# Kernel optimization log

Hardware: AMD Instinct MI355X
Metric: run time of the kernel (lower is better)

## Reference

```python
import jax, jax.numpy as jnp
import numpy as np

N = 100_000   # nodes
E = 1_280_000 # edges
F_IN = 64
HID = 64

def setup_inputs() -> dict:
    key = jax.random.key(0)
    ks = jax.random.split(key, 5)
    x = jax.random.normal(ks[0], (N, F_IN), dtype=jnp.float32)
    edge_index = jax.random.randint(ks[1], (2, E), 0, N, dtype=jnp.int32)
    edge_weight = jax.random.uniform(ks[2], (E,), dtype=jnp.float32)
    s1 = 1.0 / np.sqrt(F_IN)
    W1 = jax.random.uniform(ks[3], (F_IN, HID), minval=-s1, maxval=s1, dtype=jnp.float32)
    b1 = jnp.zeros((HID,), jnp.float32)
    s2 = 1.0 / np.sqrt(HID)
    W2 = jax.random.uniform(ks[4], (HID, 1), minval=-s2, maxval=s2, dtype=jnp.float32)
    b2 = jnp.zeros((1,), jnp.float32)
    return {"x": x, "edge_index": edge_index, "edge_weight": edge_weight,
            "W1": W1, "b1": b1, "W2": W2, "b2": b2}


def reference(x, edge_index, edge_weight, W1, b1, W2, b2):
    # eval mode: edge dropout and feature dropout are identity.
    # GCNConv with add_self_loops=True: A_hat = A + I, D_hat^-1/2 A_hat D_hat^-1/2.
    row, col = edge_index[0], edge_index[1]
    sl = jnp.arange(N, dtype=row.dtype)
    row = jnp.concatenate([row, sl])
    col = jnp.concatenate([col, sl])
    w = jnp.concatenate([edge_weight, jnp.ones((N,), edge_weight.dtype)])
    # symmetric normalization (shared by both conv layers)
    deg = jax.ops.segment_sum(w, col, num_segments=N)          # [N]
    dinv = jnp.where(deg > 0, jax.lax.rsqrt(deg), 0.0)
    norm = dinv[row] * w * dinv[col]                           # [E+N]

    def gcn(h):  # h: [N, d] already linearly transformed
        msg = h[row] * norm[:, None]                           # gather + scale
        return jax.ops.segment_sum(msg, col, num_segments=N)   # scatter-add

    h = gcn(x @ W1) + b1          # conv1
    h = jax.nn.relu(h)            # relu (dropout = identity in eval)
    out = gcn(h @ W2) + b2        # conv2 -> [N, 1]
    return out
```

## Files before the change

kernel.cpp:

```cpp
#include <hip/hip_runtime.h>
#include <hip/hip_fp16.h>

#define CNT_SHIFT 26
#define DEG_MASK  ((1u << CNT_SHIFT) - 1)
#define DEG_SCALE 1048576.0f
#define CAP 8192
#define GSTRIDE 16

typedef __attribute__((ext_vector_type(8))) short short8;
typedef __attribute__((ext_vector_type(4))) float v4f;

__device__ __forceinline__ unsigned short f_to_h16(float f) {
    return __half_as_ushort(__float2half(f));
}
__device__ __forceinline__ float h16_to_f(unsigned short u) {
    return __half2float(__ushort_as_half(u));
}
__device__ __forceinline__ unsigned short f_to_bf16(float f) {
    unsigned int u = __float_as_uint(f);
    u += 0x7fffu + ((u >> 16) & 1u);
    return (unsigned short)(u >> 16);
}
__device__ __forceinline__ unsigned long long mkrec(int r, int c, float wv) {
    return (unsigned long long)r | ((unsigned long long)(c & 511) << 17)
         | ((unsigned long long)f_to_h16(wv) << 26);
}

__global__ __launch_bounds__(256) void k_scatter_gemm(
        const int4* __restrict__ row4, const int4* __restrict__ col4, const float4* __restrict__ w4,
        const int* __restrict__ row, const int* __restrict__ col, const float* __restrict__ w,
        unsigned* __restrict__ gcur, unsigned long long* __restrict__ binrec,
        const float* __restrict__ x, const float* __restrict__ W1,
        char* __restrict__ h1q, float* __restrict__ scales,
        int E4, int rem, int nBlkE, int nGemm, int n, int nbkt) {
    __shared__ int h[256];
    int blk = blockIdx.x, t = threadIdx.x;
    if (blk < nBlkE) {
        h[t] = 0;
        __syncthreads();
        int base = blk * 1024;
#pragma unroll
        for (int k = 0; k < 4; ++k) {
            int g = base + k * 256 + t;
            if (g < E4) {
                int4 c = col4[g];
                atomicAdd(&h[c.x >> 9], 1);
                atomicAdd(&h[c.y >> 9], 1);
                atomicAdd(&h[c.z >> 9], 1);
                atomicAdd(&h[c.w >> 9], 1);
            }
        }
        if (blk == 0 && t < rem) atomicAdd(&h[col[4 * E4 + t] >> 9], 1);
        __syncthreads();
        if (t < nbkt) {
            int bb = t + (blk % nbkt);
            bb -= (bb >= nbkt) ? nbkt : 0;
            int cnt = h[bb];
            int runbase = 0;
            if (cnt > 0) runbase = (int)atomicAdd(&gcur[(size_t)bb * GSTRIDE], (unsigned)cnt);
            h[bb] = bb * CAP + runbase;
        }
        __syncthreads();
#pragma unroll
        for (int k = 0; k < 4; ++k) {
            int g = base + k * 256 + t;
            if (g < E4) {
                int4   r = row4[g];
                int4   c = col4[g];
                float4 v = w4[g];
                { int pos = atomicAdd(&h[c.x >> 9], 1); binrec[pos] = mkrec(r.x, c.x, v.x); }
                { int pos = atomicAdd(&h[c.y >> 9], 1); binrec[pos] = mkrec(r.y, c.y, v.y); }
                { int pos = atomicAdd(&h[c.z >> 9], 1); binrec[pos] = mkrec(r.z, c.z, v.z); }
                { int pos = atomicAdd(&h[c.w >> 9], 1); binrec[pos] = mkrec(r.w, c.w, v.w); }
            }
        }
        if (blk == 0 && t < rem) {
            int e = 4 * E4 + t;
            int c = col[e];
            int pos = atomicAdd(&h[c >> 9], 1);
            binrec[pos] = mkrec(row[e], c, w[e]);
        }
    } else {
        int b = blk - nBlkE;
        int lane = t & 63;
        int wave = t >> 6;
        int q   = lane >> 4;
        int n16 = lane & 15;
        short8 bf[8];
#pragma unroll
        for (int ct = 0; ct < 4; ++ct) {
#pragma unroll
            for (int hh = 0; hh < 2; ++hh) {
                short8 v;
#pragma unroll
                for (int j = 0; j < 8; ++j)
                    v[j] = (short)f_to_bf16(W1[(hh * 32 + q * 8 + j) * 64 + ct * 16 + n16]);
                bf[ct * 2 + hh] = v;
            }
        }
        int ntile = (n + 15) >> 4;
        int stride = nGemm * 4;
        for (int tile = b * 4 + wave; tile < ntile; tile += stride) {
            int base = tile << 4;
            short8 a0, a1;
            if (base + 16 <= n) {
                const float* xr = x + (size_t)(base + n16) * 64 + q * 8;
                float4 u0 = *(const float4*)(xr);
                float4 u1 = *(const float4*)(xr + 4);
                float4 u2 = *(const float4*)(xr + 32);
                float4 u3 = *(const float4*)(xr + 36);
                a0[0] = (short)f_to_bf16(u0.x); a0[1] = (short)f_to_bf16(u0.y);
                a0[2] = (short)f_to_bf16(u0.z); a0[3] = (short)f_to_bf16(u0.w);
                a0[4] = (short)f_to_bf16(u1.x); a0[5] = (short)f_to_bf16(u1.y);
                a0[6] = (short)f_to_bf16(u1.z); a0[7] = (short)f_to_bf16(u1.w);
                a1[0] = (short)f_to_bf16(u2.x); a1[1] = (short)f_to_bf16(u2.y);
                a1[2] = (short)f_to_bf16(u2.z); a1[3] = (short)f_to_bf16(u2.w);
                a1[4] = (short)f_to_bf16(u3.x); a1[5] = (short)f_to_bf16(u3.y);
                a1[6] = (short)f_to_bf16(u3.z); a1[7] = (short)f_to_bf16(u3.w);
            } else {
                bool ok = (base + n16) < n;
                const float* xr = x + (size_t)(ok ? (base + n16) : 0) * 64 + q * 8;
#pragma unroll
                for (int j = 0; j < 8; ++j) {
                    a0[j] = ok ? (short)f_to_bf16(xr[j])      : (short)0;
                    a1[j] = ok ? (short)f_to_bf16(xr[32 + j]) : (short)0;
                }
            }
            v4f acc0 = {0.f, 0.f, 0.f, 0.f}, acc1 = acc0, acc2 = acc0, acc3 = acc0;
            acc0 = __builtin_amdgcn_mfma_f32_16x16x32_bf16(a0, bf[0], acc0, 0, 0, 0);
            acc0 = __builtin_amdgcn_mfma_f32_16x16x32_bf16(a1, bf[1], acc0, 0, 0, 0);
            acc1 = __builtin_amdgcn_mfma_f32_16x16x32_bf16(a0, bf[2], acc1, 0, 0, 0);
            acc1 = __builtin_amdgcn_mfma_f32_16x16x32_bf16(a1, bf[3], acc1, 0, 0, 0);
            acc2 = __builtin_amdgcn_mfma_f32_16x16x32_bf16(a0, bf[4], acc2, 0, 0, 0);
            acc2 = __builtin_amdgcn_mfma_f32_16x16x32_bf16(a1, bf[5], acc2, 0, 0, 0);
            acc3 = __builtin_amdgcn_mfma_f32_16x16x32_bf16(a0, bf[6], acc3, 0, 0, 0);
            acc3 = __builtin_amdgcn_mfma_f32_16x16x32_bf16(a1, bf[7], acc3, 0, 0, 0);
#pragma unroll
            for (int r = 0; r < 4; ++r) {
                int rowg = base + q * 4 + r;
                if (rowg >= n) break;
                float m = fmaxf(fmaxf(fabsf(acc0[r]), fabsf(acc1[r])),
                                fmaxf(fabsf(acc2[r]), fabsf(acc3[r])));
                m = fmaxf(m, __shfl_xor(m, 1, 64));
                m = fmaxf(m, __shfl_xor(m, 2, 64));
                m = fmaxf(m, __shfl_xor(m, 4, 64));
                m = fmaxf(m, __shfl_xor(m, 8, 64));
                m = fmaxf(m, 1e-20f);
                float inv = 127.0f / m;
                char* dst = h1q + (size_t)rowg * 64 + n16;
                dst[0]  = (char)__float2int_rn(acc0[r] * inv);
                dst[16] = (char)__float2int_rn(acc1[r] * inv);
                dst[32] = (char)__float2int_rn(acc2[r] * inv);
                dst[48] = (char)__float2int_rn(acc3[r] * inv);
                if (n16 == 0) scales[rowg] = m * (1.0f / 127.0f);
            }
        }
    }
}

__global__ __launch_bounds__(256) void k_bucket(
        const unsigned long long* __restrict__ binrec, const unsigned* __restrict__ gcur,
        float* __restrict__ dinv, int* __restrict__ off, int* __restrict__ bktend,
        unsigned* __restrict__ ep, float* __restrict__ scales,
        int N, int nbkt) {
    __shared__ unsigned cnt[512];
    __shared__ int   loff[512];
    __shared__ int   ssum[256];
    int b = blockIdx.x, t = threadIdx.x;
    int e0 = b * CAP;
    int tot = (int)gcur[(size_t)b * GSTRIDE];
    int e1 = e0 + tot;
    cnt[t] = 0u; cnt[t + 256] = 0u;
    __syncthreads();
    unsigned epw[32];
    unsigned crk[32];
#pragma unroll
    for (int k = 0; k < 32; ++k) {
        int i = e0 + t + k * 256;
        if (i < e1) {
            unsigned long long rec = binrec[i];
            int cl = (int)((rec >> 17) & 511);
            unsigned hb = (unsigned)((rec >> 26) & 0xFFFF);
            float wv = h16_to_f((unsigned short)hb);
            unsigned old = atomicAdd(&cnt[cl],
                                     (1u << CNT_SHIFT) + (unsigned)(wv * DEG_SCALE + 0.5f));
            unsigned rank = old >> CNT_SHIFT;
            epw[k] = ((unsigned)(rec & 0x1FFFF) << 15) | (hb & 0x7fffu);
            crk[k] = ((unsigned)cl << 16) | rank;
        }
    }
    __syncthreads();
    unsigned p0 = cnt[2 * t], p1 = cnt[2 * t + 1];
    int c0 = (int)(p0 >> CNT_SHIFT), c1 = (int)(p1 >> CNT_SHIFT);
    float d0 = rsqrtf((float)(p0 & DEG_MASK) * (1.0f / DEG_SCALE) + 1.0f);
    float d1 = rsqrtf((float)(p1 & DEG_MASK) * (1.0f / DEG_SCALE) + 1.0f);
    int ps = c0 + c1;
    ssum[t] = ps;
    __syncthreads();
    for (int o = 1; o < 256; o <<= 1) {
        int v = (t >= o) ? ssum[t - o] : 0;
        __syncthreads();
        ssum[t] += v;
        __syncthreads();
    }
    int excl = ssum[t] - ps;
    loff[2 * t] = excl;
    loff[2 * t + 1] = excl + c0;
    int id0 = (b << 9) + 2 * t, id1 = id0 + 1;
    if (id0 < N) { dinv[id0] = d0; scales[id0] *= d0; off[id0] = e0 + excl; }
    if (id1 < N) { dinv[id1] = d1; scales[id1] *= d1; off[id1] = e0 + excl + c0; }
    if (t == 0) bktend[b] = e1;
    __syncthreads();
#pragma unroll
    for (int k = 0; k < 32; ++k) {
        int i = e0 + t + k * 256;
        if (i < e1) {
            int cl   = (int)(crk[k] >> 16);
            int rank = (int)(crk[k] & 0xFFFFu);
            ep[e0 + loff[cl] + rank] = epw[k];
        }
    }
}

__global__ __launch_bounds__(256) void k_agg1(
        const char* __restrict__ h1q, const float* __restrict__ scales,
        const int* __restrict__ off, const int* __restrict__ bktend,
        const unsigned* __restrict__ ep,
        const float* __restrict__ dinv, const float* __restrict__ b1,
        const float* __restrict__ W2,
        float* __restrict__ h2, int n) {
    int lane = threadIdx.x & 63;
    int wave = threadIdx.x >> 6;
    int grp  = lane >> 4;
    int fl   = (lane & 15) * 4;
    int i = blockIdx.x * 4 + wave;
    if (i >= n) return;
    float di = dinv[i];
    float4 acc;
    {
        char4 q4 = *(const char4*)(h1q + (size_t)i * 64 + fl);
        float si = (grp == 0) ? scales[i] : 0.f;
        acc.x = (float)q4.x * si;
        acc.y = (float)q4.y * si;
        acc.z = (float)q4.z * si;
        acc.w = (float)q4.w * si;
    }
    int s = off[i];
    int s1 = (((i & 511) == 511) || (i == n - 1)) ? bktend[i >> 9] : off[i + 1];
    for (; s + 8 <= s1; s += 8) {
        unsigned ea = ep[s + grp];
        unsigned eb = ep[s + 4 + grp];
        const char4 qa = *(const char4*)(h1q + (size_t)(ea >> 15) * 64 + fl);
        const char4 qb = *(const char4*)(h1q + (size_t)(eb >> 15) * 64 + fl);
        float ma = scales[ea >> 15] * h16_to_f((unsigned short)(ea & 0x7fff));
        float mb = scales[eb >> 15] * h16_to_f((unsigned short)(eb & 0x7fff));
        acc.x = fmaf((float)qa.x, ma, acc.x);
        acc.y = fmaf((float)qa.y, ma, acc.y);
        acc.z = fmaf((float)qa.z, ma, acc.z);
        acc.w = fmaf((float)qa.w, ma, acc.w);
        acc.x = fmaf((float)qb.x, mb, acc.x);
        acc.y = fmaf((float)qb.y, mb, acc.y);
        acc.z = fmaf((float)qb.z, mb, acc.z);
        acc.w = fmaf((float)qb.w, mb, acc.w);
    }
    for (; s < s1; s += 4) {
        int idx = s + grp;
        int sI = (idx < s1) ? idx : (s1 - 1);
        unsigned e = ep[sI];
        float m = (idx < s1) ? scales[e >> 15] * h16_to_f((unsigned short)(e & 0x7fff)) : 0.f;
        const char4 q4 = *(const char4*)(h1q + (size_t)(e >> 15) * 64 + fl);
        acc.x = fmaf((float)q4.x, m, acc.x);
        acc.y = fmaf((float)q4.y, m, acc.y);
        acc.z = fmaf((float)q4.z, m, acc.z);
        acc.w = fmaf((float)q4.w, m, acc.w);
    }
    acc.x += __shfl_xor(acc.x, 16, 64); acc.x += __shfl_xor(acc.x, 32, 64);
    acc.y += __shfl_xor(acc.y, 16, 64); acc.y += __shfl_xor(acc.y, 32, 64);
    acc.z += __shfl_xor(acc.z, 16, 64); acc.z += __shfl_xor(acc.z, 32, 64);
    acc.w += __shfl_xor(acc.w, 16, 64); acc.w += __shfl_xor(acc.w, 32, 64);
    float4 bb = *(const float4*)(b1 + fl);
    float4 ww = *(const float4*)(W2 + fl);
    float p = fmaxf(fmaf(di, acc.x, bb.x), 0.f) * ww.x
            + fmaxf(fmaf(di, acc.y, bb.y), 0.f) * ww.y
            + fmaxf(fmaf(di, acc.z, bb.z), 0.f) * ww.z
            + fmaxf(fmaf(di, acc.w, bb.w), 0.f) * ww.w;
#pragma unroll
    for (int o = 1; o < 16; o <<= 1) p += __shfl_xor(p, o, 64);
    if (lane == 0) h2[i] = di * p;
}

__global__ void k_agg2(const float* __restrict__ h2,
                       const int* __restrict__ off, const int* __restrict__ bktend,
                       const unsigned* __restrict__ ep, const float* __restrict__ dinv,
                       const float* __restrict__ b2, float* __restrict__ out, int n) {
    int i = blockIdx.x * 256 + threadIdx.x;
    if (i >= n) return;
    float acc = h2[i];
    int s = off[i];
    int s1 = (((i & 511) == 511) || (i == n - 1)) ? bktend[i >> 9] : off[i + 1];
    for (; s + 8 <= s1; s += 8) {
        unsigned e0 = ep[s],     e1 = ep[s + 1], e2 = ep[s + 2], e3 = ep[s + 3];
        unsigned e4 = ep[s + 4], e5 = ep[s + 5], e6 = ep[s + 6], e7 = ep[s + 7];
        float v0 = h2[e0 >> 15], v1 = h2[e1 >> 15], v2 = h2[e2 >> 15], v3 = h2[e3 >> 15];
        float v4 = h2[e4 >> 15], v5 = h2[e5 >> 15], v6 = h2[e6 >> 15], v7 = h2[e7 >> 15];
        acc = fmaf(v0, h16_to_f((unsigned short)(e0 & 0x7fff)), acc);
        acc = fmaf(v1, h16_to_f((unsigned short)(e1 & 0x7fff)), acc);
        acc = fmaf(v2, h16_to_f((unsigned short)(e2 & 0x7fff)), acc);
        acc = fmaf(v3, h16_to_f((unsigned short)(e3 & 0x7fff)), acc);
        acc = fmaf(v4, h16_to_f((unsigned short)(e4 & 0x7fff)), acc);
        acc = fmaf(v5, h16_to_f((unsigned short)(e5 & 0x7fff)), acc);
        acc = fmaf(v6, h16_to_f((unsigned short)(e6 & 0x7fff)), acc);
        acc = fmaf(v7, h16_to_f((unsigned short)(e7 & 0x7fff)), acc);
    }
    for (; s + 4 <= s1; s += 4) {
        unsigned e0 = ep[s], e1 = ep[s + 1], e2 = ep[s + 2], e3 = ep[s + 3];
        float v0 = h2[e0 >> 15], v1 = h2[e1 >> 15], v2 = h2[e2 >> 15], v3 = h2[e3 >> 15];
        acc = fmaf(v0, h16_to_f((unsigned short)(e0 & 0x7fff)), acc);
        acc = fmaf(v1, h16_to_f((unsigned short)(e1 & 0x7fff)), acc);
        acc = fmaf(v2, h16_to_f((unsigned short)(e2 & 0x7fff)), acc);
        acc = fmaf(v3, h16_to_f((unsigned short)(e3 & 0x7fff)), acc);
    }
    for (; s < s1; ++s) {
        unsigned e = ep[s];
        acc = fmaf(h2[e >> 15], h16_to_f((unsigned short)(e & 0x7fff)), acc);
    }
    out[i] = dinv[i] * acc + b2[0];
}

extern "C" void kernel_launch(void* const* d_in, const int* in_sizes, int n_in,
                              void* d_out, int out_size, void* d_ws, size_t ws_size,
                              hipStream_t stream) {
    const float* x  = (const float*)d_in[0];
    const int*   ei = (const int*)d_in[1];
    const float* w  = (const float*)d_in[2];
    const float* W1 = (const float*)d_in[3];
    const float* b1 = (const float*)d_in[4];
    const float* W2 = (const float*)d_in[5];
    const float* b2 = (const float*)d_in[6];
    float* out = (float*)d_out;

    const int N = in_sizes[0] / 64;
    const int E = in_sizes[2];
    const int* row = ei;
    const int* col = ei + E;

    const int nbkt  = (N + 511) >> 9;
    const int E4    = E / 4;
    const int rem   = E - 4 * E4;
    const int nBlkE = (E4 + 1023) / 1024;
    const int nGemm = 1024;

    char* p = (char*)d_ws;
    auto take = [&](size_t bytes) { char* q = p; p += (bytes + 15) & ~(size_t)15; return q; };
    unsigned long long* binrec = (unsigned long long*)take((size_t)nbkt * CAP * 8);
    unsigned* gcur = (unsigned*)take((size_t)nbkt * GSTRIDE * 4);
    int* bktend  = (int*)take((size_t)nbkt * 4);
    char* h1q    = (char*)take((size_t)N * 64);
    float* scales= (float*)take((size_t)N * 4);
    float* dinv  = (float*)take((size_t)N * 4);
    int*   off   = (int*)take((size_t)(N + 1) * 4);
    unsigned* ep = (unsigned*)take((size_t)nbkt * CAP * 4);
    float* h2    = (float*)take((size_t)N * 4);

    (void)hipMemsetAsync(gcur, 0, (size_t)nbkt * GSTRIDE * 4, stream);
    k_scatter_gemm<<<nBlkE + nGemm, 256, 0, stream>>>(
        (const int4*)row, (const int4*)col, (const float4*)w,
        row, col, w, gcur, binrec, x, W1, h1q, scales,
        E4, rem, nBlkE, nGemm, N, nbkt);
    k_bucket<<<nbkt, 256, 0, stream>>>(binrec, gcur, dinv, off, bktend, ep, scales, N, nbkt);
    k_agg1<<<(N + 3) / 4, 256, 0, stream>>>(h1q, scales, off, bktend, ep, dinv, b1, W2, h2, N);
    k_agg2<<<(N + 255) / 256, 256, 0, stream>>>(h2, off, bktend, ep, dinv, b2, out, N);
}
```

Measured before the change: 183.7 us.

## Stage edge records in LDS per wave and use offset-uint8 features in agg1

Switches the quantized hidden features to offset-binary uint8 (value+128), so agg1 can unpack them with shifts and masks and subtract a 128*sum(weights) correction once at the end. The edge loop now loads up to 64 edge records per wave cooperatively, computes each edge's scale times weight once, and stores source index plus multiplier in shared memory, then gathers features in groups of 8. This removes the redundant per-lane ep and scales loads done by all 16 lanes of each group and shortens the tail handling. In exchange it adds LDS traffic, an extra running sum, and a possible cancellation error from the offset correction.

```diff
diff --git a/kernel.cpp b/kernel.cpp
--- a/kernel.cpp
+++ b/kernel.cpp
@@ -147,11 +147,11 @@
                 m = fmaxf(m, __shfl_xor(m, 8, 64));
                 m = fmaxf(m, 1e-20f);
                 float inv = 127.0f / m;
-                char* dst = h1q + (size_t)rowg * 64 + n16;
-                dst[0]  = (char)__float2int_rn(acc0[r] * inv);
-                dst[16] = (char)__float2int_rn(acc1[r] * inv);
-                dst[32] = (char)__float2int_rn(acc2[r] * inv);
-                dst[48] = (char)__float2int_rn(acc3[r] * inv);
+                unsigned char* dst = (unsigned char*)h1q + (size_t)rowg * 64 + n16;
+                dst[0]  = (unsigned char)(__float2int_rn(acc0[r] * inv) + 128);
+                dst[16] = (unsigned char)(__float2int_rn(acc1[r] * inv) + 128);
+                dst[32] = (unsigned char)(__float2int_rn(acc2[r] * inv) + 128);
+                dst[48] = (unsigned char)(__float2int_rn(acc3[r] * inv) + 128);
                 if (n16 == 0) scales[rowg] = m * (1.0f / 127.0f);
             }
         }
@@ -223,12 +223,14 @@
 }
 
 __global__ __launch_bounds__(256) void k_agg1(
-        const char* __restrict__ h1q, const float* __restrict__ scales,
+        const char* __restrict__ h1q_, const float* __restrict__ scales,
         const int* __restrict__ off, const int* __restrict__ bktend,
         const unsigned* __restrict__ ep,
         const float* __restrict__ dinv, const float* __restrict__ b1,
         const float* __restrict__ W2,
         float* __restrict__ h2, int n) {
+    const unsigned char* __restrict__ h1q = (const unsigned char*)h1q_;
+    __shared__ uint2 tbl[4][64];
     int lane = threadIdx.x & 63;
     int wave = threadIdx.x >> 6;
     int grp  = lane >> 4;
@@ -236,48 +238,58 @@
     int i = blockIdx.x * 4 + wave;
     if (i >= n) return;
     float di = dinv[i];
+    int s  = off[i];
+    int s1 = (((i & 511) == 511) || (i == n - 1)) ? bktend[i >> 9] : off[i + 1];
+
     float4 acc;
+    float S;
     {
-        char4 q4 = *(const char4*)(h1q + (size_t)i * 64 + fl);
+        unsigned q4 = *(const unsigned*)(h1q + (size_t)i * 64 + fl);
         float si = (grp == 0) ? scales[i] : 0.f;
-        acc.x = (float)q4.x * si;
-        acc.y = (float)q4.y * si;
-        acc.z = (float)q4.z * si;
-        acc.w = (float)q4.w * si;
-    }
-    int s = off[i];
-    int s1 = (((i & 511) == 511) || (i == n - 1)) ? bktend[i >> 9] : off[i + 1];
-    for (; s + 8 <= s1; s += 8) {
-        unsigned ea = ep[s + grp];
-        unsigned eb = ep[s + 4 + grp];
-        const char4 qa = *(const char4*)(h1q + (size_t)(ea >> 15) * 64 + fl);
-        const char4 qb = *(const char4*)(h1q + (size_t)(eb >> 15) * 64 + fl);
-        float ma = scales[ea >> 15] * h16_to_f((unsigned short)(ea & 0x7fff));
-        float mb = scales[eb >> 15] * h16_to_f((unsigned short)(eb & 0x7fff));
-        acc.x = fmaf((float)qa.x, ma, acc.x);
-        acc.y = fmaf((float)qa.y, ma, acc.y);
-        acc.z = fmaf((float)qa.z, ma, acc.z);
-        acc.w = fmaf((float)qa.w, ma, acc.w);
-        acc.x = fmaf((float)qb.x, mb, acc.x);
-        acc.y = fmaf((float)qb.y, mb, acc.y);
-        acc.z = fmaf((float)qb.z, mb, acc.z);
-        acc.w = fmaf((float)qb.w, mb, acc.w);
-    }
-    for (; s < s1; s += 4) {
-        int idx = s + grp;
-        int sI = (idx < s1) ? idx : (s1 - 1);
-        unsigned e = ep[sI];
-        float m = (idx < s1) ? scales[e >> 15] * h16_to_f((unsigned short)(e & 0x7fff)) : 0.f;
-        const char4 q4 = *(const char4*)(h1q + (size_t)(e >> 15) * 64 + fl);
-        acc.x = fmaf((float)q4.x, m, acc.x);
-        acc.y = fmaf((float)q4.y, m, acc.y);
-        acc.z = fmaf((float)q4.z, m, acc.z);
-        acc.w = fmaf((float)q4.w, m, acc.w);
+        acc.x = (float)(q4 & 0xffu)         * si;
+        acc.y = (float)((q4 >> 8) & 0xffu)  * si;
+        acc.z = (float)((q4 >> 16) & 0xffu) * si;
+        acc.w = (float)(q4 >> 24)           * si;
+        S = si;
+    }
+    for (int c0 = s; c0 < s1; c0 += 64) {
+        int cl = s1 - c0; if (cl > 64) cl = 64;
+        {
+            unsigned src = 0u; float m = 0.f;
+            if (lane < cl) {
+                unsigned e = ep[c0 + lane];
+                src = e >> 15;
+                m = scales[src] * h16_to_f((unsigned short)(e & 0x7fff));
+            }
+            tbl[wave][lane] = make_uint2(src, __float_as_uint(m));
+        }
+        for (int j0 = 0; j0 < cl; j0 += 8) {
+            uint2 ta = tbl[wave][j0 + grp];
+            uint2 tb = tbl[wave][j0 + 4 + grp];
+            float ma = __uint_as_float(ta.y);
+            float mb = __uint_as_float(tb.y);
+            unsigned qa = *(const unsigned*)(h1q + ((size_t)ta.x << 6) + fl);
+            unsigned qb = *(const unsigned*)(h1q + ((size_t)tb.x << 6) + fl);
+            acc.x = fmaf((float)(qa & 0xffu),         ma, acc.x);
+            acc.y = fmaf((float)((qa >> 8) & 0xffu),  ma, acc.y);
+            acc.z = fmaf((float)((qa >> 16) & 0xffu), ma, acc.z);
+            acc.w = fmaf((float)(qa >> 24),           ma, acc.w);
+            acc.x = fmaf((float)(qb & 0xffu),         mb, acc.x);
+            acc.y = fmaf((float)((qb >> 8) & 0xffu),  mb, acc.y);
+            acc.z = fmaf((float)((qb >> 16) & 0xffu), mb, acc.z);
+            acc.w = fmaf((float)(qb >> 24),           mb, acc.w);
+            S += ma + mb;
+        }
     }
     acc.x += __shfl_xor(acc.x, 16, 64); acc.x += __shfl_xor(acc.x, 32, 64);
     acc.y += __shfl_xor(acc.y, 16, 64); acc.y += __shfl_xor(acc.y, 32, 64);
     acc.z += __shfl_xor(acc.z, 16, 64); acc.z += __shfl_xor(acc.z, 32, 64);
     acc.w += __shfl_xor(acc.w, 16, 64); acc.w += __shfl_xor(acc.w, 32, 64);
+    S += __shfl_xor(S, 16, 64); S += __shfl_xor(S, 32, 64);
+    acc.x = fmaf(S, -128.f, acc.x);
+    acc.y = fmaf(S, -128.f, acc.y);
+    acc.z = fmaf(S, -128.f, acc.z);
+    acc.w = fmaf(S, -128.f, acc.w);
     float4 bb = *(const float4*)(b1 + fl);
     float4 ww = *(const float4*)(W2 + fl);
     float p = fmaxf(fmaf(di, acc.x, bb.x), 0.f) * ww.x
```

Result: faster. 174.8 us (-4.9%).
